# Kernel optimization log

Measured on AMD Instinct MI355X. Metric: run time of the kernel, lower is better.

## Reference

```python
import jax, jax.numpy as jnp
import numpy as np

B, T, D = 4, 2048, 1024
H, HD = 16, 64  # n_heads, head_dim; H*HD == D

def setup_inputs() -> dict:
    key = jax.random.key(0)
    ks = jax.random.split(key, 9)
    s = 1.0 / np.sqrt(D)
    return {
        "x": jax.random.normal(ks[0], (B, T, D), dtype=jnp.float32),
        "Wq": jax.random.normal(ks[1], (D, D), dtype=jnp.float32) * s,
        "bq": jnp.zeros((D,), dtype=jnp.float32),
        "Wk": jax.random.normal(ks[2], (D, D), dtype=jnp.float32) * s,
        "bk": jnp.zeros((D,), dtype=jnp.float32),
        "Wv": jax.random.normal(ks[3], (D, D), dtype=jnp.float32) * s,
        "bv": jnp.zeros((D,), dtype=jnp.float32),
        "Wo": jax.random.normal(ks[4], (D, D), dtype=jnp.float32) * s,
        "bo": jnp.zeros((D,), dtype=jnp.float32),
    }

def reference(x, Wq, bq, Wk, bk, Wv, bv, Wo, bo):
    # Linear(in,out): y = x @ W.T + b (weights stored [out,in])
    q = (jnp.einsum('btd,ed->bte', x, Wq) + bq).reshape(B, T, H, HD).transpose(0, 2, 1, 3)
    k = (jnp.einsum('btd,ed->bte', x, Wk) + bk).reshape(B, T, H, HD).transpose(0, 2, 1, 3)
    v = (jnp.einsum('btd,ed->bte', x, Wv) + bv).reshape(B, T, H, HD).transpose(0, 2, 1, 3)
    scale = jnp.sqrt(jnp.asarray(HD, dtype=x.dtype))
    attn = jnp.einsum('bhqd,bhkd->bhqk', q, k) / scale  # [B,H,T,T]
    attn = jax.nn.softmax(attn, axis=-1)
    out = jnp.einsum('bhqk,bhkd->bhqd', attn, v)
    out = out.transpose(0, 2, 1, 3).reshape(B, T, H * HD)
    return jnp.einsum('bte,de->btd', out, Wo) + bo
```

## Files before the change

kernel.cpp:

```cpp
#include <hip/hip_runtime.h>
#include <hip/hip_bf16.h>

#define B_ 4
#define T_ 2048
#define D_ 1024
#define H_ 16
#define HD_ 64
#define M_ (B_ * T_)

typedef __attribute__((ext_vector_type(8))) short   s16x8;
typedef __attribute__((ext_vector_type(4))) short   s16x4;
typedef __attribute__((ext_vector_type(4))) float   f32x4;
typedef __attribute__((ext_vector_type(4))) float   fvec4;
typedef __attribute__((ext_vector_type(4))) unsigned short u16x4;

union U4 { u16x4 v; unsigned int w[2]; };
union P8 { s16x8 v; unsigned int w[4]; };

__device__ inline unsigned int pk_bf16(float a, float b) {
    unsigned int r;
    asm("v_cvt_pk_bf16_f32 %0, %1, %2" : "=v"(r) : "v"(a), "v"(b));
    return r;
}

__device__ inline f32x4 mfma32(s16x8 a, s16x8 b, f32x4 c) {
    return __builtin_amdgcn_mfma_f32_16x16x32_bf16(a, b, c, 0, 0, 0);
}

__device__ inline void gld16(const unsigned short* g, unsigned short* l) {
    __builtin_amdgcn_global_load_lds(
        (const __attribute__((address_space(1))) unsigned int*)g,
        (__attribute__((address_space(3))) unsigned int*)l, 16, 0, 0);
}

__global__ void cvt_all(const float* __restrict__ x,
                        const float* __restrict__ wq, const float* __restrict__ wk,
                        const float* __restrict__ wv, const float* __restrict__ wo,
                        unsigned short* __restrict__ xb, unsigned short* __restrict__ wcat) {
    const int bid = blockIdx.x;
    const float* src; unsigned short* dst; int off;
    if (bid < 8192)       { src = x;  dst = xb;                  off = bid; }
    else if (bid < 9216)  { src = wq; dst = wcat;                off = bid - 8192; }
    else if (bid < 10240) { src = wk; dst = wcat + 1 * 1048576;  off = bid - 9216; }
    else if (bid < 11264) { src = wv; dst = wcat + 2 * 1048576;  off = bid - 10240; }
    else                  { src = wo; dst = wcat + 3 * 1048576;  off = bid - 11264; }
    int i = off * 1024 + threadIdx.x * 4;
    fvec4 v = *(const fvec4*)(src + i);
    U4 o;
    o.w[0] = pk_bf16(v[0], v[1]);
    o.w[1] = pk_bf16(v[2], v[3]);
    *(u16x4*)(dst + i) = o.v;
}

__device__ __forceinline__ void gemm_core(
    const unsigned short* __restrict__ P0, const unsigned short* __restrict__ P1,
    int o0, int o1, int tid, unsigned short* As, unsigned short* Bs,
    f32x4 acc[4][4]) {
    const int lane = tid & 63, wave = tid >> 6;
    const int quad = lane >> 4, l16 = lane & 15;
    const int wr = (wave >> 1) * 64, wc = (wave & 1) * 64;
    const int sxo = (quad ^ ((l16 >> 1) & 3)) * 8;

    const int row0 = tid >> 2;
    const int c8 = ((tid & 3) ^ ((tid >> 3) & 3)) * 8;
    const unsigned short* gA0 = P0 + (size_t)(o0 + row0) * 1024 + c8;
    const unsigned short* gA1 = gA0 + 64 * 1024;
    const unsigned short* gB0 = P1 + (size_t)(o1 + row0) * 1024 + c8;
    const unsigned short* gB1 = gB0 + 64 * 1024;
    unsigned short* dA = As + tid * 8;
    unsigned short* dB = Bs + tid * 8;

    const unsigned short* rA = As + (wr + l16) * 32 + sxo;
    const unsigned short* rB = Bs + (wc + l16) * 32 + sxo;

#define STG(buf_, kn_) do {                                   \
        gld16(gA0 + (kn_), dA + (buf_) * 4096);               \
        gld16(gA1 + (kn_), dA + (buf_) * 4096 + 2048);        \
        gld16(gB0 + (kn_), dB + (buf_) * 4096);               \
        gld16(gB1 + (kn_), dB + (buf_) * 4096 + 2048);        \
    } while (0)

    STG(0, 0);
    STG(1, 32);

#pragma unroll
    for (int c = 0; c < 32; ++c) {
        if (c < 31) { asm volatile("s_waitcnt vmcnt(4)" ::: "memory"); }
        else        { asm volatile("s_waitcnt vmcnt(0)" ::: "memory"); }
        __builtin_amdgcn_s_barrier();
        if (c + 2 < 32) { STG((c + 2) % 3, (c + 2) * 32); }
        const int rb = c % 3;
        s16x8 af[4], bfr[4];
        for (int i = 0; i < 4; ++i)
            af[i] = *(const s16x8*)(rA + rb * 4096 + i * 512);
        for (int j = 0; j < 4; ++j)
            bfr[j] = *(const s16x8*)(rB + rb * 4096 + j * 512);
        __builtin_amdgcn_s_setprio(1);
        for (int i = 0; i < 4; ++i)
            for (int j = 0; j < 4; ++j)
                acc[i][j] = mfma32(af[i], bfr[j], acc[i][j]);
        __builtin_amdgcn_s_setprio(0);
    }
#undef STG
}

__global__ __launch_bounds__(256) void gemm_qkv(
    const unsigned short* __restrict__ A, const unsigned short* __restrict__ Wcat,
    const float* __restrict__ bq, const float* __restrict__ bk, const float* __restrict__ bv,
    unsigned short* __restrict__ Qb, unsigned short* __restrict__ Kb,
    unsigned short* __restrict__ Vt, float qscale) {
    __shared__ __align__(16) unsigned short As[3 * 4096];
    __shared__ __align__(16) unsigned short Bs[3 * 4096];
    const int flat = blockIdx.x;
    const int j = flat >> 3;
    const int mt = (flat & 7) * 8 + (j & 7);
    const int y  = j >> 3;
    const int proj = y >> 3;
    const int m0 = mt * 128, n0 = (y & 7) * 128;
    const unsigned short* W = Wcat + (size_t)proj * 1048576;
    const float* bias = proj == 0 ? bq : (proj == 1 ? bk : bv);

    const int tid = threadIdx.x;
    const int lane = tid & 63, wave = tid >> 6;
    const int quad = lane >> 4, l16 = lane & 15;
    const int wr = (wave >> 1) * 64, wc = (wave & 1) * 64;

    f32x4 acc[4][4] = {};

    if (proj != 2) {
        gemm_core(W, A, n0, m0, tid, As, Bs, acc);
        const float scale = (proj == 0) ? qscale : 1.0f;
        unsigned short* outp = (proj == 0) ? Qb : Kb;
        for (int jj = 0; jj < 4; ++jj) {
            int t = m0 + wc + jj * 16 + l16;
            int b = t >> 11, tt = t & (T_ - 1);
            for (int i = 0; i < 4; ++i) {
                int nb = n0 + wr + i * 16 + quad * 4;
                fvec4 bi = *(const fvec4*)(bias + nb);
                int h = nb >> 6, hd = nb & 63;
                float v0 = (acc[i][jj][0] + bi[0]) * scale;
                float v1 = (acc[i][jj][1] + bi[1]) * scale;
                float v2 = (acc[i][jj][2] + bi[2]) * scale;
                float v3 = (acc[i][jj][3] + bi[3]) * scale;
                U4 o;
                o.w[0] = pk_bf16(v0, v1);
                o.w[1] = pk_bf16(v2, v3);
                *(u16x4*)(outp + ((size_t)(b * H_ + h) * T_ + tt) * HD_ + hd) = o.v;
            }
        }
    } else {
        gemm_core(A, W, m0, n0, tid, As, Bs, acc);
        for (int i = 0; i < 4; ++i) {
            int mbase = m0 + wr + i * 16 + quad * 4;
            int b = mbase >> 11, t = mbase & (T_ - 1);
            int tp = (t & ~31) | (((t >> 2) & 3) << 3) | (((t >> 4) & 1) << 2);
            for (int jj = 0; jj < 4; ++jj) {
                int n = n0 + wc + jj * 16 + l16;
                float bi = bias[n];
                int h = n >> 6, hd = n & 63;
                U4 o;
                o.w[0] = pk_bf16(acc[i][jj][0] + bi, acc[i][jj][1] + bi);
                o.w[1] = pk_bf16(acc[i][jj][2] + bi, acc[i][jj][3] + bi);
                *(u16x4*)(Vt + ((size_t)(b * H_ + h) * HD_ + hd) * T_ + tp) = o.v;
            }
        }
    }
}

__global__ __launch_bounds__(256) void gemm_o(
    const unsigned short* __restrict__ A, const unsigned short* __restrict__ W,
    const float* __restrict__ bias, float* __restrict__ out) {
    __shared__ __align__(16) unsigned short As[3 * 4096];
    __shared__ __align__(16) unsigned short Bs[3 * 4096];
    const int flat = blockIdx.x;
    const int j = flat >> 3;
    const int m0 = ((flat & 7) * 8 + (j & 7)) * 128;
    const int n0 = (j >> 3) * 128;

    const int tid = threadIdx.x;
    const int lane = tid & 63, wave = tid >> 6;
    const int quad = lane >> 4, l16 = lane & 15;
    const int wr = (wave >> 1) * 64, wc = (wave & 1) * 64;

    f32x4 acc[4][4] = {};
    gemm_core(W, A, n0, m0, tid, As, Bs, acc);

    for (int jj = 0; jj < 4; ++jj) {
        int m = m0 + wc + jj * 16 + l16;
        for (int i = 0; i < 4; ++i) {
            int nb = n0 + wr + i * 16 + quad * 4;
            fvec4 bi = *(const fvec4*)(bias + nb);
            fvec4 o = acc[i][jj] + bi;
            *(fvec4*)(out + (size_t)m * D_ + nb) = o;
        }
    }
}

__global__ __launch_bounds__(256) void attn(
    const unsigned short* __restrict__ Qb, const unsigned short* __restrict__ Kb,
    const unsigned short* __restrict__ Vt, unsigned short* __restrict__ Ob) {
    __shared__ __align__(16) unsigned short Ks[2 * 4096];
    __shared__ __align__(16) unsigned short Vs[2 * 4096];

    const int tid = threadIdx.x;
    const int wave = tid >> 6, lane = tid & 63;
    const int quad = lane >> 4, l16 = lane & 15;

    const int flat = blockIdx.y * 16 + blockIdx.x;
    const int wid  = (flat & 7) * 128 + (flat >> 3);
    const int qblk = wid & 15, bh = wid >> 4;
    const int b = bh >> 4, h = bh & 15;
    const int q0 = qblk * 128 + wave * 32;

    const unsigned short* Qp = Qb + (size_t)bh * T_ * HD_;
    const unsigned short* Kp = Kb + (size_t)bh * T_ * HD_;
    const unsigned short* Vp = Vt + (size_t)bh * HD_ * T_;

    s16x8 qf[2][2];
    for (int qt = 0; qt < 2; ++qt)
        for (int ds = 0; ds < 2; ++ds)
            qf[qt][ds] = *(const s16x8*)(Qp + (size_t)(q0 + qt * 16 + l16) * HD_ + ds * 32 + quad * 8);

    f32x4 accO[2][4] = {};
    f32x4 accL[2] = {};
    const f32x4 fzero = {0.f, 0.f, 0.f, 0.f};

    const s16x8 ones = {0x3F80, 0x3F80, 0x3F80, 0x3F80,
                        0x3F80, 0x3F80, 0x3F80, 0x3F80};

    const int r0 = tid >> 3,           cg0 = (tid & 7) ^ (r0 & 7);
    const int r1 = (tid + 256) >> 3,   cg1 = (tid & 7) ^ (r1 & 7);

    const unsigned short* kp0 = Kp + (size_t)r0 * HD_ + cg0 * 8;
    const unsigned short* kp1 = Kp + (size_t)r1 * HD_ + cg1 * 8;
    const unsigned short* vp0 = Vp + (size_t)r0 * T_ + cg0 * 8;
    const unsigned short* vp1 = Vp + (size_t)r1 * T_ + cg1 * 8;

    const int xk   = quad ^ (l16 & 7);
    const int kro  = l16 * 64 + xk * 8;
    const int kro1 = l16 * 64 + (xk ^ 4) * 8;
    const int vro0 = l16 * 64 + ((quad)     ^ (l16 & 7)) * 8;
    const int vro1 = l16 * 64 + ((4 + quad) ^ (l16 & 7)) * 8;

    gld16(kp0, Ks + tid * 8);  gld16(kp1, Ks + tid * 8 + 2048);
    gld16(vp0, Vs + tid * 8);  gld16(vp1, Vs + tid * 8 + 2048);
    kp0 += 64 * HD_; kp1 += 64 * HD_; vp0 += 64; vp1 += 64;

#pragma unroll 2
    for (int c = 0; c < T_ / 64; ++c) {
        __syncthreads();

        if (c + 1 < T_ / 64) {
            unsigned short* dK = Ks + ((c + 1) & 1) * 4096 + tid * 8;
            unsigned short* dV = Vs + ((c + 1) & 1) * 4096 + tid * 8;
            gld16(kp0, dK);  gld16(kp1, dK + 2048);
            gld16(vp0, dV);  gld16(vp1, dV + 2048);
            kp0 += 64 * HD_; kp1 += 64 * HD_; vp0 += 64; vp1 += 64;
        }

        const unsigned short* Kc = Ks + (c & 1) * 4096;
        const unsigned short* Vc = Vs + (c & 1) * 4096;

        f32x4 st[2][4];
        __builtin_amdgcn_s_setprio(1);
        for (int kt = 0; kt < 4; ++kt) {
            s16x8 kf0 = *(const s16x8*)(Kc + kt * 1024 + kro);
            s16x8 kf1 = *(const s16x8*)(Kc + kt * 1024 + kro1);
            st[0][kt] = mfma32(kf0, qf[0][0], fzero);
            st[0][kt] = mfma32(kf1, qf[0][1], st[0][kt]);
            st[1][kt] = mfma32(kf0, qf[1][0], fzero);
            st[1][kt] = mfma32(kf1, qf[1][1], st[1][kt]);
        }
        __builtin_amdgcn_s_setprio(0);

        s16x8 pf[2][2];
        for (int qt = 0; qt < 2; ++qt)
            for (int u = 0; u < 2; ++u) {
                P8 pk;
                for (int kk = 0; kk < 2; ++kk) {
                    f32x4 s = st[qt][2 * u + kk];
                    float p0 = __builtin_amdgcn_exp2f(s[0]);
                    float p1 = __builtin_amdgcn_exp2f(s[1]);
                    float p2 = __builtin_amdgcn_exp2f(s[2]);
                    float p3 = __builtin_amdgcn_exp2f(s[3]);
                    pk.w[2 * kk]     = pk_bf16(p0, p1);
                    pk.w[2 * kk + 1] = pk_bf16(p2, p3);
                }
                pf[qt][u] = pk.v;
            }

        __builtin_amdgcn_s_setprio(1);
        accL[0] = mfma32(ones, pf[0][0], accL[0]);
        accL[1] = mfma32(ones, pf[1][0], accL[1]);
        for (int dt = 0; dt < 4; ++dt) {
            s16x8 vf = *(const s16x8*)(Vc + vro0 + dt * 1024);
            accO[0][dt] = mfma32(vf, pf[0][0], accO[0][dt]);
            accO[1][dt] = mfma32(vf, pf[1][0], accO[1][dt]);
        }
        accL[0] = mfma32(ones, pf[0][1], accL[0]);
        accL[1] = mfma32(ones, pf[1][1], accL[1]);
        for (int dt = 0; dt < 4; ++dt) {
            s16x8 vf = *(const s16x8*)(Vc + vro1 + dt * 1024);
            accO[0][dt] = mfma32(vf, pf[0][1], accO[0][dt]);
            accO[1][dt] = mfma32(vf, pf[1][1], accO[1][dt]);
        }
        __builtin_amdgcn_s_setprio(0);
    }

    for (int qt = 0; qt < 2; ++qt) {
        float inv = 1.f / accL[qt][0];
        int t = q0 + qt * 16 + l16;
        for (int dt = 0; dt < 4; ++dt) {
            U4 o;
            o.w[0] = pk_bf16(accO[qt][dt][0] * inv, accO[qt][dt][1] * inv);
            o.w[1] = pk_bf16(accO[qt][dt][2] * inv, accO[qt][dt][3] * inv);
            *(u16x4*)(Ob + ((size_t)b * T_ + t) * D_ + h * 64 + dt * 16 + quad * 4) = o.v;
        }
    }
}

extern "C" void kernel_launch(void* const* d_in, const int* in_sizes, int n_in,
                              void* d_out, int out_size, void* d_ws, size_t ws_size,
                              hipStream_t stream) {
    const float* x  = (const float*)d_in[0];
    const float* Wq = (const float*)d_in[1];
    const float* bq = (const float*)d_in[2];
    const float* Wk = (const float*)d_in[3];
    const float* bk = (const float*)d_in[4];
    const float* Wv = (const float*)d_in[5];
    const float* bv = (const float*)d_in[6];
    const float* Wo = (const float*)d_in[7];
    const float* bo = (const float*)d_in[8];
    float* out = (float*)d_out;

    const size_t SZ = (size_t)M_ * D_ * sizeof(unsigned short);
    unsigned short* xb   = (unsigned short*)d_ws;
    unsigned short* Qb   = (unsigned short*)((char*)d_ws + 1 * SZ);
    unsigned short* Kb   = (unsigned short*)((char*)d_ws + 2 * SZ);
    unsigned short* Vbt  = (unsigned short*)((char*)d_ws + 3 * SZ);
    unsigned short* Wcat = (unsigned short*)((char*)d_ws + 4 * SZ);
    unsigned short* Ob   = xb;

    const float qscale = 1.4426950408889634f / 8.0f;

    dim3 blk(256);
    cvt_all<<<dim3(12288), blk, 0, stream>>>(x, Wq, Wk, Wv, Wo, xb, Wcat);
    gemm_qkv<<<dim3(1536), blk, 0, stream>>>(xb, Wcat, bq, bk, bv, Qb, Kb, Vbt, qscale);
    attn<<<dim3(T_ / 128, B_ * H_), blk, 0, stream>>>(Qb, Kb, Vbt, Ob);
    gemm_o<<<dim3(512), blk, 0, stream>>>(Ob, Wcat + 3 * 1048576, bo, out);
}
```

Baseline: 273.0 us.

## Double attention query tile per wave and deepen K/V pipeline to four buffers

Each wave now handles 64 query rows instead of 32, so every K/V fragment read from shared memory feeds twice as many MFMAs, and the grid shrinks to 512 blocks. The K/V staging becomes a 4-deep ring with prefetch distance 2, fenced by explicit vmcnt waits and raw barriers instead of __syncthreads. Launch bounds now request 2 blocks per CU. The cost is more registers for accumulators and Q fragments, twice the LDS per block (64 KB), and fewer blocks to spread across CUs.

Result: faster. 254.5 us (median of 2 runs) (-6.8%).

```diff
diff --git a/kernel.cpp b/kernel.cpp
--- a/kernel.cpp
+++ b/kernel.cpp
@@ -196,33 +196,33 @@
     }
 }
 
-__global__ __launch_bounds__(256) void attn(
+__global__ __launch_bounds__(256, 2) void attn(
     const unsigned short* __restrict__ Qb, const unsigned short* __restrict__ Kb,
     const unsigned short* __restrict__ Vt, unsigned short* __restrict__ Ob) {
-    __shared__ __align__(16) unsigned short Ks[2 * 4096];
-    __shared__ __align__(16) unsigned short Vs[2 * 4096];
+    __shared__ __align__(16) unsigned short Ks[4 * 4096];
+    __shared__ __align__(16) unsigned short Vs[4 * 4096];
 
     const int tid = threadIdx.x;
     const int wave = tid >> 6, lane = tid & 63;
     const int quad = lane >> 4, l16 = lane & 15;
 
-    const int flat = blockIdx.y * 16 + blockIdx.x;
-    const int wid  = (flat & 7) * 128 + (flat >> 3);
-    const int qblk = wid & 15, bh = wid >> 4;
+    const int flat = blockIdx.x;
+    const int wid  = (flat & 7) * 64 + (flat >> 3);
+    const int qblk = wid & 7, bh = wid >> 3;
     const int b = bh >> 4, h = bh & 15;
-    const int q0 = qblk * 128 + wave * 32;
+    const int q0 = qblk * 256 + wave * 64;
 
     const unsigned short* Qp = Qb + (size_t)bh * T_ * HD_;
     const unsigned short* Kp = Kb + (size_t)bh * T_ * HD_;
     const unsigned short* Vp = Vt + (size_t)bh * HD_ * T_;
 
-    s16x8 qf[2][2];
-    for (int qt = 0; qt < 2; ++qt)
+    s16x8 qf[4][2];
+    for (int qt = 0; qt < 4; ++qt)
         for (int ds = 0; ds < 2; ++ds)
             qf[qt][ds] = *(const s16x8*)(Qp + (size_t)(q0 + qt * 16 + l16) * HD_ + ds * 32 + quad * 8);
 
-    f32x4 accO[2][4] = {};
-    f32x4 accL[2] = {};
+    f32x4 accO[4][4] = {};
+    f32x4 accL[4] = {};
     const f32x4 fzero = {0.f, 0.f, 0.f, 0.f};
 
     const s16x8 ones = {0x3F80, 0x3F80, 0x3F80, 0x3F80,
@@ -235,6 +235,9 @@
     const unsigned short* kp1 = Kp + (size_t)r1 * HD_ + cg1 * 8;
     const unsigned short* vp0 = Vp + (size_t)r0 * T_ + cg0 * 8;
     const unsigned short* vp1 = Vp + (size_t)r1 * T_ + cg1 * 8;
+
+    unsigned short* dK0 = Ks + tid * 8;
+    unsigned short* dV0 = Vs + tid * 8;
 
     const int xk   = quad ^ (l16 & 7);
     const int kro  = l16 * 64 + xk * 8;
@@ -242,72 +245,85 @@
     const int vro0 = l16 * 64 + ((quad)     ^ (l16 & 7)) * 8;
     const int vro1 = l16 * 64 + ((4 + quad) ^ (l16 & 7)) * 8;
 
-    gld16(kp0, Ks + tid * 8);  gld16(kp1, Ks + tid * 8 + 2048);
-    gld16(vp0, Vs + tid * 8);  gld16(vp1, Vs + tid * 8 + 2048);
-    kp0 += 64 * HD_; kp1 += 64 * HD_; vp0 += 64; vp1 += 64;
-
-#pragma unroll 2
-    for (int c = 0; c < T_ / 64; ++c) {
-        __syncthreads();
-
-        if (c + 1 < T_ / 64) {
-            unsigned short* dK = Ks + ((c + 1) & 1) * 4096 + tid * 8;
-            unsigned short* dV = Vs + ((c + 1) & 1) * 4096 + tid * 8;
-            gld16(kp0, dK);  gld16(kp1, dK + 2048);
-            gld16(vp0, dV);  gld16(vp1, dV + 2048);
-            kp0 += 64 * HD_; kp1 += 64 * HD_; vp0 += 64; vp1 += 64;
-        }
-
-        const unsigned short* Kc = Ks + (c & 1) * 4096;
-        const unsigned short* Vc = Vs + (c & 1) * 4096;
-
-        f32x4 st[2][4];
-        __builtin_amdgcn_s_setprio(1);
-        for (int kt = 0; kt < 4; ++kt) {
-            s16x8 kf0 = *(const s16x8*)(Kc + kt * 1024 + kro);
-            s16x8 kf1 = *(const s16x8*)(Kc + kt * 1024 + kro1);
-            st[0][kt] = mfma32(kf0, qf[0][0], fzero);
-            st[0][kt] = mfma32(kf1, qf[0][1], st[0][kt]);
-            st[1][kt] = mfma32(kf0, qf[1][0], fzero);
-            st[1][kt] = mfma32(kf1, qf[1][1], st[1][kt]);
-        }
-        __builtin_amdgcn_s_setprio(0);
-
-        s16x8 pf[2][2];
-        for (int qt = 0; qt < 2; ++qt)
-            for (int u = 0; u < 2; ++u) {
+    auto STAGE = [&](int bufi) {
+        gld16(kp0, dK0 + bufi * 4096);  gld16(kp1, dK0 + bufi * 4096 + 2048);
+        gld16(vp0, dV0 + bufi * 4096);  gld16(vp1, dV0 + bufi * 4096 + 2048);
+        kp0 += 64 * HD_; kp1 += 64 * HD_; vp0 += 64; vp1 += 64;
+    };
+
+    auto CHUNK = [&](int bufi) {
+        const unsigned short* Kc = Ks + bufi * 4096;
+        const unsigned short* Vc = Vs + bufi * 4096;
+#pragma unroll
+        for (int u = 0; u < 2; ++u) {
+            f32x4 st[4][2];
+            __builtin_amdgcn_s_setprio(1);
+#pragma unroll
+            for (int kt2 = 0; kt2 < 2; ++kt2) {
+                const int kt = 2 * u + kt2;
+                s16x8 kf0 = *(const s16x8*)(Kc + kt * 1024 + kro);
+                s16x8 kf1 = *(const s16x8*)(Kc + kt * 1024 + kro1);
+                for (int qt = 0; qt < 4; ++qt) {
+                    st[qt][kt2] = mfma32(kf0, qf[qt][0], fzero);
+                    st[qt][kt2] = mfma32(kf1, qf[qt][1], st[qt][kt2]);
+                }
+            }
+            __builtin_amdgcn_s_setprio(0);
+            s16x8 pf[4];
+            for (int qt = 0; qt < 4; ++qt) {
                 P8 pk;
-                for (int kk = 0; kk < 2; ++kk) {
-                    f32x4 s = st[qt][2 * u + kk];
+#pragma unroll
+                for (int kt2 = 0; kt2 < 2; ++kt2) {
+                    f32x4 s = st[qt][kt2];
                     float p0 = __builtin_amdgcn_exp2f(s[0]);
                     float p1 = __builtin_amdgcn_exp2f(s[1]);
                     float p2 = __builtin_amdgcn_exp2f(s[2]);
                     float p3 = __builtin_amdgcn_exp2f(s[3]);
-                    pk.w[2 * kk]     = pk_bf16(p0, p1);
-                    pk.w[2 * kk + 1] = pk_bf16(p2, p3);
+                    pk.w[2 * kt2]     = pk_bf16(p0, p1);
+                    pk.w[2 * kt2 + 1] = pk_bf16(p2, p3);
                 }
-                pf[qt][u] = pk.v;
-            }
-
-        __builtin_amdgcn_s_setprio(1);
-        accL[0] = mfma32(ones, pf[0][0], accL[0]);
-        accL[1] = mfma32(ones, pf[1][0], accL[1]);
-        for (int dt = 0; dt < 4; ++dt) {
-            s16x8 vf = *(const s16x8*)(Vc + vro0 + dt * 1024);
-            accO[0][dt] = mfma32(vf, pf[0][0], accO[0][dt]);
-            accO[1][dt] = mfma32(vf, pf[1][0], accO[1][dt]);
-        }
-        accL[0] = mfma32(ones, pf[0][1], accL[0]);
-        accL[1] = mfma32(ones, pf[1][1], accL[1]);
-        for (int dt = 0; dt < 4; ++dt) {
-            s16x8 vf = *(const s16x8*)(Vc + vro1 + dt * 1024);
-            accO[0][dt] = mfma32(vf, pf[0][1], accO[0][dt]);
-            accO[1][dt] = mfma32(vf, pf[1][1], accO[1][dt]);
-        }
-        __builtin_amdgcn_s_setprio(0);
-    }
-
-    for (int qt = 0; qt < 2; ++qt) {
+                pf[qt] = pk.v;
+            }
+            __builtin_amdgcn_s_setprio(1);
+            for (int qt = 0; qt < 4; ++qt)
+                accL[qt] = mfma32(ones, pf[qt], accL[qt]);
+            const int vro = (u == 0) ? vro0 : vro1;
+            for (int dt = 0; dt < 4; ++dt) {
+                s16x8 vf = *(const s16x8*)(Vc + vro + dt * 1024);
+                for (int qt = 0; qt < 4; ++qt)
+                    accO[qt][dt] = mfma32(vf, pf[qt], accO[qt][dt]);
+            }
+            __builtin_amdgcn_s_setprio(0);
+        }
+    };
+
+    STAGE(0);
+    STAGE(1);
+
+#pragma nounroll
+    for (int cc = 0; cc < 28; cc += 4) {
+#pragma unroll
+        for (int k = 0; k < 4; ++k) {
+            asm volatile("s_waitcnt vmcnt(4)" ::: "memory");
+            __builtin_amdgcn_s_barrier();
+            STAGE((k + 2) & 3);
+            CHUNK(k);
+        }
+    }
+    asm volatile("s_waitcnt vmcnt(4)" ::: "memory");
+    __builtin_amdgcn_s_barrier();
+    STAGE(2); CHUNK(0);
+    asm volatile("s_waitcnt vmcnt(4)" ::: "memory");
+    __builtin_amdgcn_s_barrier();
+    STAGE(3); CHUNK(1);
+    asm volatile("s_waitcnt vmcnt(4)" ::: "memory");
+    __builtin_amdgcn_s_barrier();
+    CHUNK(2);
+    asm volatile("s_waitcnt vmcnt(0)" ::: "memory");
+    __builtin_amdgcn_s_barrier();
+    CHUNK(3);
+
+    for (int qt = 0; qt < 4; ++qt) {
         float inv = 1.f / accL[qt][0];
         int t = q0 + qt * 16 + l16;
         for (int dt = 0; dt < 4; ++dt) {
@@ -346,6 +362,6 @@
     dim3 blk(256);
     cvt_all<<<dim3(12288), blk, 0, stream>>>(x, Wq, Wk, Wv, Wo, xb, Wcat);
     gemm_qkv<<<dim3(1536), blk, 0, stream>>>(xb, Wcat, bq, bk, bv, Qb, Kb, Vbt, qscale);
-    attn<<<dim3(T_ / 128, B_ * H_), blk, 0, stream>>>(Qb, Kb, Vbt, Ob);
+    attn<<<dim3(512), blk, 0, stream>>>(Qb, Kb, Vbt, Ob);
     gemm_o<<<dim3(512), blk, 0, stream>>>(Ob, Wcat + 3 * 1048576, bo, out);
 }
```
